# Kernel optimization log

Hardware: AMD Instinct MI355X
Metric: run time of the kernel (lower is better)

## Reference

```python
import jax, jax.numpy as jnp
import numpy as np

IN_DIM = 2048
OUT_DIM = 1536
N_PARAM = max(IN_DIM, OUT_DIM)  # 2048


def setup_inputs() -> dict:
    key = jax.random.key(0)
    k1, k2, k3 = jax.random.split(key, 3)
    x = jax.random.normal(k1, (8, 64, 64, IN_DIM), dtype=jnp.float32)
    # NOTE: original init is zeros for W_first_col (output would be all-zero);
    # we use randn so the reference computes something non-trivial.
    W_first_col = jax.random.normal(k2, (N_PARAM,), dtype=jnp.float32)
    W_second_col = jax.random.normal(k3, (N_PARAM,), dtype=jnp.float32)
    return {"x": x, "W_first_col": W_first_col, "W_second_col": W_second_col}


def reference(x, W_first_col, W_second_col):
    # Effective first column of the circulant matrix, truncated to in_dim
    W = (W_first_col * W_second_col)[:IN_DIM]            # [C]
    W_fft = jnp.fft.fft(W)                               # [C] complex64
    x_fft = jnp.fft.fft(x, axis=-1)                      # [B,H,W,C] complex64
    result = jnp.fft.ifft(W_fft * x_fft, axis=-1).real   # circular conv along channels
    return result[..., :OUT_DIM]                         # [B,H,W,out_dim]
```

## Files before the change

### kernel.cpp

```cpp
#include <hip/hip_runtime.h>
#include <math.h>

#define C_LEN 2048
#define HALF  1024
#define OUTD  1536
#define NPIX  32768

__device__ __forceinline__ int SWZ(int idx) { return idx ^ ((idx >> 5) & 31); }

template<int DIR>
__device__ void fft2048(float* r0, float* i0, float* r1, float* i1, int t) {
    float *sr = r0, *si = i0, *dr = r1, *di = i1;
    const float TW = (float)DIR * 6.283185307179586f / 2048.0f;
    const float FD = (float)DIR;
    __syncthreads();
    #pragma unroll
    for (int b = 0; b < 4; ++b) {
        int t2 = t + b * 256;
        float ar = sr[SWZ(t2)],        ai = si[SWZ(t2)];
        float br = sr[SWZ(t2 + 1024)], bi = si[SWZ(t2 + 1024)];
        float sn, cs;
        sincosf(TW * (float)t2, &sn, &cs);
        float vr = ar - br, vi = ai - bi;
        int w0 = 2 * t2;
        dr[SWZ(w0)]     = ar + br;
        di[SWZ(w0)]     = ai + bi;
        dr[SWZ(w0 + 1)] = cs * vr - sn * vi;
        di[SWZ(w0 + 1)] = cs * vi + sn * vr;
    }
    { float* tp; tp = sr; sr = dr; dr = tp; tp = si; si = di; di = tp; }
    #pragma unroll
    for (int m = 2; m <= 512; m *= 4) {
        __syncthreads();
        #pragma unroll
        for (int b = 0; b < 2; ++b) {
            int t2 = t + b * 256;
            int jm = t2 & ~(m - 1);
            float a0r = sr[SWZ(t2)],        a0i = si[SWZ(t2)];
            float a1r = sr[SWZ(t2 + 512)],  a1i = si[SWZ(t2 + 512)];
            float a2r = sr[SWZ(t2 + 1024)], a2i = si[SWZ(t2 + 1024)];
            float a3r = sr[SWZ(t2 + 1536)], a3i = si[SWZ(t2 + 1536)];
            float s0r = a0r + a2r, s0i = a0i + a2i;
            float d0r = a0r - a2r, d0i = a0i - a2i;
            float s1r = a1r + a3r, s1i = a1i + a3i;
            float d1r = a1r - a3r, d1i = a1i - a3i;
            float A0r = s0r + s1r, A0i = s0i + s1i;
            float A2r = s0r - s1r, A2i = s0i - s1i;
            float A1r = d0r - FD * d1i, A1i = d0i + FD * d1r;
            float A3r = d0r + FD * d1i, A3i = d0i - FD * d1r;
            float s1w, c1w;
            sincosf(TW * (float)jm, &s1w, &c1w);
            float c2w = c1w * c1w - s1w * s1w, s2w = 2.0f * c1w * s1w;
            float c3w = c1w * c2w - s1w * s2w, s3w = c1w * s2w + s1w * c2w;
            int wb = t2 + 3 * jm;
            dr[SWZ(wb)]         = A0r;
            di[SWZ(wb)]         = A0i;
            dr[SWZ(wb + m)]     = c1w * A1r - s1w * A1i;
            di[SWZ(wb + m)]     = c1w * A1i + s1w * A1r;
            dr[SWZ(wb + 2 * m)] = c2w * A2r - s2w * A2i;
            di[SWZ(wb + 2 * m)] = c2w * A2i + s2w * A2r;
            dr[SWZ(wb + 3 * m)] = c3w * A3r - s3w * A3i;
            di[SWZ(wb + 3 * m)] = c3w * A3i + s3w * A3r;
        }
        { float* tp; tp = sr; sr = dr; dr = tp; tp = si; si = di; di = tp; }
    }
    __syncthreads();
}

__global__ __launch_bounds__(256)
void uv_kernel(const float* __restrict__ w1, const float* __restrict__ w2,
               float4* __restrict__ uv) {
    __shared__ float r0[C_LEN], i0[C_LEN], r1[C_LEN], i1[C_LEN];
    int t = threadIdx.x;
    #pragma unroll
    for (int k = 0; k < 8; ++k) {
        int e = t + k * 256;
        r0[SWZ(e)] = w1[e] * w2[e];
        i0[SWZ(e)] = 0.0f;
    }
    fft2048<-1>(r0, i0, r1, i1, t);
    #pragma unroll
    for (int b = 0; b < 4; ++b) {
        int k = t + b * 256;
        float w1r = r0[SWZ(k)],        w1i = i0[SWZ(k)];
        float w2r = r0[SWZ(k + 1024)], w2i = i0[SWZ(k + 1024)];
        float Sr = (w1r + w2r) * (1.0f / 4096.0f);
        float Si = (w1i + w2i) * (1.0f / 4096.0f);
        float Dr = (w1r - w2r) * (1.0f / 4096.0f);
        float Di = (w1i - w2i) * (1.0f / 4096.0f);
        float sn, cs;
        sincosf((6.283185307179586f / 2048.0f) * (float)k, &sn, &cs);
        float Er = cs * Dr - sn * Di, Ei = cs * Di + sn * Dr;
        float Fr = cs * Dr + sn * Di, Fi = cs * Di - sn * Dr;
        uv[k] = make_float4(Sr - Ei, Si + Er, Sr + Fi, Si - Fr);
    }
}

__device__ __forceinline__ void cm(float& or_, float& oi_, float ar, float ai,
                                   float br, float bi) {
    or_ = ar * br - ai * bi;
    oi_ = ar * bi + ai * br;
}

template<int S>
__device__ __forceinline__ void fft16_ip(float* xr, float* xi) {
    const float FS = (float)S;
    const float C1 = 0.9238795325112867f;
    const float S1 = 0.3826834323650898f;
    const float R2 = 0.7071067811865476f;
    #pragma unroll
    for (int n0 = 0; n0 < 4; ++n0) {
        float a0r = xr[n0],      a0i = xi[n0];
        float a1r = xr[n0 + 4],  a1i = xi[n0 + 4];
        float a2r = xr[n0 + 8],  a2i = xi[n0 + 8];
        float a3r = xr[n0 + 12], a3i = xi[n0 + 12];
        float t0r = a0r + a2r, t0i = a0i + a2i;
        float t1r = a0r - a2r, t1i = a0i - a2i;
        float t2r = a1r + a3r, t2i = a1i + a3i;
        float t3r = a1r - a3r, t3i = a1i - a3i;
        float y1r = t1r - FS * t3i, y1i = t1i + FS * t3r;
        float y2r = t0r - t2r,      y2i = t0i - t2i;
        float y3r = t1r + FS * t3i, y3i = t1i - FS * t3r;
        xr[n0] = t0r + t2r;  xi[n0] = t0i + t2i;
        if (n0 == 0) {
            xr[4]  = y1r; xi[4]  = y1i;
            xr[8]  = y2r; xi[8]  = y2i;
            xr[12] = y3r; xi[12] = y3i;
        } else if (n0 == 1) {
            cm(xr[5],  xi[5],  y1r, y1i, C1,  FS * S1);
            cm(xr[9],  xi[9],  y2r, y2i, R2,  FS * R2);
            cm(xr[13], xi[13], y3r, y3i, S1,  FS * C1);
        } else if (n0 == 2) {
            cm(xr[6],  xi[6],  y1r, y1i, R2,  FS * R2);
            xr[10] = -FS * y2i;  xi[10] = FS * y2r;
            cm(xr[14], xi[14], y3r, y3i, -R2, FS * R2);
        } else {
            cm(xr[7],  xi[7],  y1r, y1i, S1,  FS * C1);
            cm(xr[11], xi[11], y2r, y2i, -R2, FS * R2);
            cm(xr[15], xi[15], y3r, y3i, -C1, -FS * S1);
        }
    }
    #pragma unroll
    for (int k0 = 0; k0 < 4; ++k0) {
        float b0r = xr[4 * k0],     b0i = xi[4 * k0];
        float b1r = xr[4 * k0 + 1], b1i = xi[4 * k0 + 1];
        float b2r = xr[4 * k0 + 2], b2i = xi[4 * k0 + 2];
        float b3r = xr[4 * k0 + 3], b3i = xi[4 * k0 + 3];
        float t0r = b0r + b2r, t0i = b0i + b2i;
        float t1r = b0r - b2r, t1i = b0i - b2i;
        float t2r = b1r + b3r, t2i = b1i + b3i;
        float t3r = b1r - b3r, t3i = b1i - b3i;
        xr[4 * k0]     = t0r + t2r;      xi[4 * k0]     = t0i + t2i;
        xr[4 * k0 + 1] = t1r - FS * t3i; xi[4 * k0 + 1] = t1i + FS * t3r;
        xr[4 * k0 + 2] = t0r - t2r;      xi[4 * k0 + 2] = t0i - t2i;
        xr[4 * k0 + 3] = t1r + FS * t3i; xi[4 * k0 + 3] = t1i - FS * t3r;
    }
}

__device__ __forceinline__ void tw_store(const float* vr, const float* vi,
                                         float2* row, int xorv, float th) {
    float bs, bc;
    __sincosf(th, &bs, &bc);
    float aR[4], aI[4], bR[4], bI[4];
    aR[0] = 1.f; aI[0] = 0.f;
    aR[1] = bc;  aI[1] = bs;
    aR[2] = bc * bc - bs * bs;          aI[2] = 2.f * bc * bs;
    aR[3] = aR[2] * bc - aI[2] * bs;    aI[3] = aR[2] * bs + aI[2] * bc;
    bR[0] = 1.f; bI[0] = 0.f;
    bR[1] = aR[2] * aR[2] - aI[2] * aI[2];  bI[1] = 2.f * aR[2] * aI[2];
    bR[2] = bR[1] * bR[1] - bI[1] * bI[1];  bI[2] = 2.f * bR[1] * bI[1];
    bR[3] = bR[2] * bR[1] - bI[2] * bI[1];  bI[3] = bR[2] * bI[1] + bI[2] * bR[1];
    #pragma unroll
    for (int c = 0; c < 16; ++c) {
        int p = ((c & 3) << 2) | (c >> 2);
        float x0 = vr[p], y0 = vi[p];
        float x1 = x0 * aR[c & 3] - y0 * aI[c & 3];
        float y1 = x0 * aI[c & 3] + y0 * aR[c & 3];
        float x2 = x1 * bR[c >> 2] - y1 * bI[c >> 2];
        float y2 = x1 * bI[c >> 2] + y1 * bR[c >> 2];
        row[c ^ xorv] = make_float2(x2, y2);
    }
}

__global__ __launch_bounds__(256, 4)
void conv256(const float* __restrict__ x, const float4* __restrict__ uv,
             float2* __restrict__ out) {
    __shared__ float2 ldsAll[4 * HALF];
    const int tid = threadIdx.x;
    const int t   = tid & 63;
    const int wid = tid >> 6;
    float2* lds = ldsAll + (wid << 10);
    const size_t pix = ((size_t)blockIdx.x << 2) + wid;
    const float2* xp = reinterpret_cast<const float2*>(x) + pix * (size_t)HALF;

    float vr[16], vi[16];
    #pragma unroll
    for (int a = 0; a < 16; ++a) {
        float2 z = xp[(a << 6) + t];
        vr[a] = z.x; vi[a] = z.y;
    }

    fft16_ip<-1>(vr, vi);
    tw_store(vr, vi, lds + (t << 4), t & 15,
             (-6.283185307179586f / 1024.0f) * (float)t);
    __syncthreads();
    {
        const int f = t & 3, c = t >> 2;
        #pragma unroll
        for (int e = 0; e < 16; ++e) {
            int row = (e << 2) + f;
            float2 z = lds[(row << 4) + (c ^ (row & 15))];
            vr[e] = z.x; vi[e] = z.y;
        }
        __syncthreads();
        fft16_ip<-1>(vr, vi);
        tw_store(vr, vi, lds + (t << 4), c,
                 (-6.283185307179586f / 64.0f) * (float)f);
    }
    __syncthreads();
    {
        const int q = t & 3, c = t >> 2;
        float dr[16], di[16];
        #pragma unroll
        for (int f = 0; f < 4; ++f) {
            #pragma unroll
            for (int s = 0; s < 4; ++s) {
                int wrow = (c << 2) + f;
                float2 z = lds[(wrow << 4) + (((q << 2) + s) ^ c)];
                dr[f * 4 + s] = z.x; di[f * 4 + s] = z.y;
            }
        }
        __syncthreads();
        #pragma unroll
        for (int s = 0; s < 4; ++s) {
            float ar = dr[0 + s],  ai = di[0 + s];
            float br = dr[4 + s],  bi = di[4 + s];
            float cr = dr[8 + s],  ci = di[8 + s];
            float er = dr[12 + s], ei = di[12 + s];
            float t0r = ar + cr, t0i = ai + ci;
            float t1r = ar - cr, t1i = ai - ci;
            float t2r = br + er, t2i = bi + ei;
            float t3r = br - er, t3i = bi - ei;
            int kb = c + (((q << 2) + s) << 4);
            lds[kb]       = make_float2(t0r + t2r, t0i + t2i);
            lds[kb + 256] = make_float2(t1r + t3i, t1i - t3r);
            lds[kb + 512] = make_float2(t0r - t2r, t0i - t2i);
            lds[kb + 768] = make_float2(t1r - t3i, t1i + t3r);
        }
    }
    __syncthreads();

    #pragma unroll
    for (int a = 0; a < 16; ++a) {
        int k = (a << 6) + t;
        float2 Za = lds[k];
        float2 Zm = lds[(HALF - k) & (HALF - 1)];
        float4 u  = uv[k];
        float Ar = Za.x + Zm.x, Ai = Za.y - Zm.y;
        float Br = Za.x - Zm.x, Bi = Za.y + Zm.y;
        vr[a] = Ar * u.x - Ai * u.y + Br * u.z - Bi * u.w;
        vi[a] = Ar * u.y + Ai * u.x + Br * u.w + Bi * u.z;
    }
    __syncthreads();

    fft16_ip<1>(vr, vi);
    tw_store(vr, vi, lds + (t << 4), t & 15,
             (6.283185307179586f / 1024.0f) * (float)t);
    __syncthreads();
    {
        const int f = t & 3, c = t >> 2;
        #pragma unroll
        for (int e = 0; e < 16; ++e) {
            int row = (e << 2) + f;
            float2 z = lds[(row << 4) + (c ^ (row & 15))];
            vr[e] = z.x; vi[e] = z.y;
        }
        __syncthreads();
        fft16_ip<1>(vr, vi);
        tw_store(vr, vi, lds + (t << 4), c,
                 (6.283185307179586f / 64.0f) * (float)f);
    }
    __syncthreads();
    {
        const int q = t & 3, c = t >> 2;
        float dr[16], di[16];
        #pragma unroll
        for (int f = 0; f < 4; ++f) {
            #pragma unroll
            for (int s = 0; s < 4; ++s) {
                int wrow = (c << 2) + f;
                float2 z = lds[(wrow << 4) + (((q << 2) + s) ^ c)];
                dr[f * 4 + s] = z.x; di[f * 4 + s] = z.y;
            }
        }
        float2* op = out + pix * (size_t)(OUTD / 2);
        #pragma unroll
        for (int s = 0; s < 4; ++s) {
            float ar = dr[0 + s],  ai = di[0 + s];
            float br = dr[4 + s],  bi = di[4 + s];
            float cr = dr[8 + s],  ci = di[8 + s];
            float er = dr[12 + s], ei = di[12 + s];
            float t0r = ar + cr, t0i = ai + ci;
            float t1r = ar - cr, t1i = ai - ci;
            float t2r = br + er, t2i = bi + ei;
            float t3r = br - er, t3i = bi - ei;
            int nb = c + (((q << 2) + s) << 4);
            op[nb]       = make_float2(t0r + t2r, t0i + t2i);
            op[nb + 256] = make_float2(t1r - t3i, t1i + t3r);
            op[nb + 512] = make_float2(t0r - t2r, t0i - t2i);
        }
    }
}

extern "C" void kernel_launch(void* const* d_in, const int* in_sizes, int n_in,
                              void* d_out, int out_size, void* d_ws, size_t ws_size,
                              hipStream_t stream) {
    const float* x  = (const float*)d_in[0];
    const float* w1 = (const float*)d_in[1];
    const float* w2 = (const float*)d_in[2];
    float2* out = (float2*)d_out;
    float4* uv  = (float4*)d_ws;

    hipLaunchKernelGGL(uv_kernel, dim3(1), dim3(256), 0, stream, w1, w2, uv);
    hipLaunchKernelGGL(conv256, dim3(NPIX / 4), dim3(256), 0, stream, x, uv, out);
}
```

Measured before the change: 144.8 us.

## Use precomputed twiddle tables and drop block barriers in wave-local FFT

Twiddle factors for the two radix-16 passes are now computed once by the setup kernel into workspace tables. The convolution kernel loads them as float4 values instead of running sincos and chained complex multiplies. Because each wavefront works only on its own LDS slice, every __syncthreads in the conv kernel is removed and the kernel relies on in-order execution within a wave. The launch bound is also raised to 8 blocks per CU. The cost is extra global and cache loads for the tables, plus reliance on wave-level ordering for LDS correctness.

```diff
diff --git a/kernel.cpp b/kernel.cpp
--- a/kernel.cpp
+++ b/kernel.cpp
@@ -69,7 +69,8 @@
 
 __global__ __launch_bounds__(256)
 void uv_kernel(const float* __restrict__ w1, const float* __restrict__ w2,
-               float4* __restrict__ uv) {
+               float4* __restrict__ uv, float2* __restrict__ tab1,
+               float2* __restrict__ tab2) {
     __shared__ float r0[C_LEN], i0[C_LEN], r1[C_LEN], i1[C_LEN];
     int t = threadIdx.x;
     #pragma unroll
@@ -93,6 +94,20 @@
         float Er = cs * Dr - sn * Di, Ei = cs * Di + sn * Dr;
         float Fr = cs * Dr + sn * Di, Fi = cs * Di - sn * Dr;
         uv[k] = make_float4(Sr - Ei, Si + Er, Sr + Fi, Si - Fr);
+    }
+    #pragma unroll
+    for (int b = 0; b < 4; ++b) {
+        int e = t + b * 256;
+        int row = e >> 4, c = e & 15;
+        float sn, cs;
+        sincosf((-6.283185307179586f / 1024.0f) * (float)(row * c), &sn, &cs);
+        tab1[e] = make_float2(cs, sn);
+    }
+    if (t < 64) {
+        int f = t >> 4, m = t & 15;
+        float sn, cs;
+        sincosf((-6.283185307179586f / 64.0f) * (float)(f * m), &sn, &cs);
+        tab2[t] = make_float2(cs, sn);
     }
 }
 
@@ -157,33 +172,31 @@
     }
 }
 
-__device__ __forceinline__ void tw_store(const float* vr, const float* vi,
-                                         float2* row, int xorv, float th) {
-    float bs, bc;
-    __sincosf(th, &bs, &bc);
-    float aR[4], aI[4], bR[4], bI[4];
-    aR[0] = 1.f; aI[0] = 0.f;
-    aR[1] = bc;  aI[1] = bs;
-    aR[2] = bc * bc - bs * bs;          aI[2] = 2.f * bc * bs;
-    aR[3] = aR[2] * bc - aI[2] * bs;    aI[3] = aR[2] * bs + aI[2] * bc;
-    bR[0] = 1.f; bI[0] = 0.f;
-    bR[1] = aR[2] * aR[2] - aI[2] * aI[2];  bI[1] = 2.f * aR[2] * aI[2];
-    bR[2] = bR[1] * bR[1] - bI[1] * bI[1];  bI[2] = 2.f * bR[1] * bI[1];
-    bR[3] = bR[2] * bR[1] - bI[2] * bI[1];  bI[3] = bR[2] * bI[1] + bI[2] * bR[1];
-    #pragma unroll
-    for (int c = 0; c < 16; ++c) {
-        int p = ((c & 3) << 2) | (c >> 2);
-        float x0 = vr[p], y0 = vi[p];
-        float x1 = x0 * aR[c & 3] - y0 * aI[c & 3];
-        float y1 = x0 * aI[c & 3] + y0 * aR[c & 3];
-        float x2 = x1 * bR[c >> 2] - y1 * bI[c >> 2];
-        float y2 = x1 * bI[c >> 2] + y1 * bR[c >> 2];
-        row[c ^ xorv] = make_float2(x2, y2);
-    }
-}
-
-__global__ __launch_bounds__(256, 4)
+template<int CONJ>
+__device__ __forceinline__ void tw_store_tab(const float* vr, const float* vi,
+                                             float2* row, int xorv,
+                                             const float2* __restrict__ tabrow) {
+    const float4* t4 = reinterpret_cast<const float4*>(tabrow);
+    #pragma unroll
+    for (int j = 0; j < 8; ++j) {
+        float4 w2v = t4[j];
+        #pragma unroll
+        for (int h = 0; h < 2; ++h) {
+            int c = 2 * j + h;
+            int p = ((c & 3) << 2) | (c >> 2);
+            float wr = h ? w2v.z : w2v.x;
+            float wi = h ? w2v.w : w2v.y;
+            if (CONJ) wi = -wi;
+            float x = vr[p] * wr - vi[p] * wi;
+            float y = vr[p] * wi + vi[p] * wr;
+            row[c ^ xorv] = make_float2(x, y);
+        }
+    }
+}
+
+__global__ __launch_bounds__(256, 8)
 void conv256(const float* __restrict__ x, const float4* __restrict__ uv,
+             const float2* __restrict__ tab1, const float2* __restrict__ tab2,
              float2* __restrict__ out) {
     __shared__ float2 ldsAll[4 * HALF];
     const int tid = threadIdx.x;
@@ -201,9 +214,7 @@
     }
 
     fft16_ip<-1>(vr, vi);
-    tw_store(vr, vi, lds + (t << 4), t & 15,
-             (-6.283185307179586f / 1024.0f) * (float)t);
-    __syncthreads();
+    tw_store_tab<0>(vr, vi, lds + (t << 4), t & 15, tab1 + (t << 4));
     {
         const int f = t & 3, c = t >> 2;
         #pragma unroll
@@ -212,12 +223,9 @@
             float2 z = lds[(row << 4) + (c ^ (row & 15))];
             vr[e] = z.x; vi[e] = z.y;
         }
-        __syncthreads();
         fft16_ip<-1>(vr, vi);
-        tw_store(vr, vi, lds + (t << 4), c,
-                 (-6.283185307179586f / 64.0f) * (float)f);
-    }
-    __syncthreads();
+        tw_store_tab<0>(vr, vi, lds + (t << 4), c, tab2 + (f << 4));
+    }
     {
         const int q = t & 3, c = t >> 2;
         float dr[16], di[16];
@@ -230,7 +238,6 @@
                 dr[f * 4 + s] = z.x; di[f * 4 + s] = z.y;
             }
         }
-        __syncthreads();
         #pragma unroll
         for (int s = 0; s < 4; ++s) {
             float ar = dr[0 + s],  ai = di[0 + s];
@@ -248,7 +255,6 @@
             lds[kb + 768] = make_float2(t1r - t3i, t1i + t3r);
         }
     }
-    __syncthreads();
 
     #pragma unroll
     for (int a = 0; a < 16; ++a) {
@@ -261,12 +267,9 @@
         vr[a] = Ar * u.x - Ai * u.y + Br * u.z - Bi * u.w;
         vi[a] = Ar * u.y + Ai * u.x + Br * u.w + Bi * u.z;
     }
-    __syncthreads();
 
     fft16_ip<1>(vr, vi);
-    tw_store(vr, vi, lds + (t << 4), t & 15,
-             (6.283185307179586f / 1024.0f) * (float)t);
-    __syncthreads();
+    tw_store_tab<1>(vr, vi, lds + (t << 4), t & 15, tab1 + (t << 4));
     {
         const int f = t & 3, c = t >> 2;
         #pragma unroll
@@ -275,12 +278,9 @@
             float2 z = lds[(row << 4) + (c ^ (row & 15))];
             vr[e] = z.x; vi[e] = z.y;
         }
-        __syncthreads();
         fft16_ip<1>(vr, vi);
-        tw_store(vr, vi, lds + (t << 4), c,
-                 (6.283185307179586f / 64.0f) * (float)f);
-    }
-    __syncthreads();
+        tw_store_tab<1>(vr, vi, lds + (t << 4), c, tab2 + (f << 4));
+    }
     {
         const int q = t & 3, c = t >> 2;
         float dr[16], di[16];
@@ -319,8 +319,13 @@
     const float* w1 = (const float*)d_in[1];
     const float* w2 = (const float*)d_in[2];
     float2* out = (float2*)d_out;
-    float4* uv  = (float4*)d_ws;
-
-    hipLaunchKernelGGL(uv_kernel, dim3(1), dim3(256), 0, stream, w1, w2, uv);
-    hipLaunchKernelGGL(conv256, dim3(NPIX / 4), dim3(256), 0, stream, x, uv, out);
-}
+    char* ws = (char*)d_ws;
+    float4* uv   = (float4*)ws;
+    float2* tab1 = (float2*)(ws + 16384);
+    float2* tab2 = (float2*)(ws + 16384 + 8192);
+
+    hipLaunchKernelGGL(uv_kernel, dim3(1), dim3(256), 0, stream,
+                       w1, w2, uv, tab1, tab2);
+    hipLaunchKernelGGL(conv256, dim3(NPIX / 4), dim3(256), 0, stream,
+                       x, uv, tab1, tab2, out);
+}
```

Result: slower. 305.0 us (+110.6%).
